# Performance work log

Measured on AMD Instinct MI355X. Metric: run time of the kernel, lower is better.

## Reference

```python
import jax, jax.numpy as jnp
import numpy as np

HEADS = 4
CH = 64  # hidden_channels (per-head out channels)
N_INT = 50000
N_LANE = 400000
E_PO = 400000
E_ADJ = 200000


def setup_inputs() -> dict:
    key = jax.random.key(0)
    ks = iter(jax.random.split(key, 32))
    rn = lambda shape, s=0.1: jax.random.normal(next(ks), shape, dtype=jnp.float32) * s
    inp = {
        'x_int': rn((N_INT, 16), 1.0),
        'x_lane': rn((N_LANE, 12), 1.0),
        'h0': jnp.zeros((N_INT, CH), jnp.float32),
        'enc_int_W': rn((16, CH)), 'enc_int_b': jnp.zeros((CH,), jnp.float32),
        'enc_lane_W': rn((12, CH)), 'enc_lane_b': jnp.zeros((CH,), jnp.float32),
        'Wsrc_po': rn((CH, HEADS * CH)), 'Wdst_po': rn((CH, HEADS * CH)),
        'att_src_po': rn((HEADS, CH)), 'att_dst_po': rn((HEADS, CH)),
        'bias_po': jnp.zeros((HEADS * CH,), jnp.float32),
        'Wsrc_adj': rn((CH, HEADS * CH)), 'Wdst_adj': rn((CH, HEADS * CH)),
        'att_src_adj': rn((HEADS, CH)), 'att_dst_adj': rn((HEADS, CH)),
        'bias_adj': jnp.zeros((HEADS * CH,), jnp.float32),
        'gru_W_ih': rn((3 * CH, HEADS * CH)), 'gru_W_hh': rn((3 * CH, CH)),
        'gru_b_ih': jnp.zeros((3 * CH,), jnp.float32), 'gru_b_hh': jnp.zeros((3 * CH,), jnp.float32),
        'W_pi': rn((CH, 8)), 'b_pi': jnp.zeros((8,), jnp.float32),
        'W_v': rn((CH, 1)), 'b_v': jnp.zeros((1,), jnp.float32),
        'src_po': jax.random.randint(next(ks), (E_PO,), 0, N_LANE),
        'dst_po': jax.random.randint(next(ks), (E_PO,), 0, N_INT),
        'src_adj': jax.random.randint(next(ks), (E_ADJ,), 0, N_INT),
        'dst_adj': jax.random.randint(next(ks), (E_ADJ,), 0, N_INT),
    }
    return inp


def gat_conv(x_src, x_dst, src, dst, Wsrc, Wdst, a_src, a_dst, bias, n_dst):
    # PyG GATConv (bipartite, concat=True, no self loops), negative_slope=0.2
    hs = (x_src @ Wsrc).reshape(-1, HEADS, CH)  # [Ns,H,C]
    hd = (x_dst @ Wdst).reshape(-1, HEADS, CH)  # [Nd,H,C]
    a_s = jnp.einsum('nhc,hc->nh', hs, a_src)   # [Ns,H]
    a_d = jnp.einsum('nhc,hc->nh', hd, a_dst)   # [Nd,H]
    alpha = jax.nn.leaky_relu(a_s[src] + a_d[dst], 0.2)        # [E,H]
    amax = jax.ops.segment_max(alpha, dst, num_segments=n_dst)  # [Nd,H]
    ex = jnp.exp(alpha - amax[dst])
    den = jax.ops.segment_sum(ex, dst, num_segments=n_dst)
    w = ex / den[dst]                                           # [E,H] softmax per dst
    msg = hs[src] * w[:, :, None]                               # [E,H,C]
    out = jax.ops.segment_sum(msg, dst, num_segments=n_dst)     # [Nd,H,C]
    return out.reshape(n_dst, HEADS * CH) + bias


def gru_cell(x, h, W_ih, W_hh, b_ih, b_hh):
    gi = x @ W_ih.T + b_ih
    gh = h @ W_hh.T + b_hh
    i_r, i_z, i_n = jnp.split(gi, 3, axis=1)
    h_r, h_z, h_n = jnp.split(gh, 3, axis=1)
    r = jax.nn.sigmoid(i_r + h_r)
    z = jax.nn.sigmoid(i_z + h_z)
    n = jnp.tanh(i_n + r * h_n)
    return (1.0 - z) * n + z * h


def reference(x_int, x_lane, h0, enc_int_W, enc_int_b, enc_lane_W, enc_lane_b,
              Wsrc_po, Wdst_po, att_src_po, att_dst_po, bias_po,
              Wsrc_adj, Wdst_adj, att_src_adj, att_dst_adj, bias_adj,
              gru_W_ih, gru_W_hh, gru_b_ih, gru_b_hh,
              W_pi, b_pi, W_v, b_v,
              src_po, dst_po, src_adj, dst_adj):
    # per-type encoders + ReLU
    e_int = jax.nn.relu(x_int @ enc_int_W + enc_int_b)    # [N_int,CH]
    e_lane = jax.nn.relu(x_lane @ enc_lane_W + enc_lane_b)  # [N_lane,CH]
    # HeteroConv aggr='sum' over relations targeting 'intersection'
    o_po = gat_conv(e_lane, e_int, src_po, dst_po, Wsrc_po, Wdst_po,
                    att_src_po, att_dst_po, bias_po, N_INT)
    o_adj = gat_conv(e_int, e_int, src_adj, dst_adj, Wsrc_adj, Wdst_adj,
                     att_src_adj, att_dst_adj, bias_adj, N_INT)
    inter = jax.nn.relu(o_po + o_adj)  # dropout = identity (deterministic eval)
    h_new = gru_cell(inter, h0, gru_W_ih, gru_W_hh, gru_b_ih, gru_b_hh)
    logits = h_new @ W_pi + b_pi
    value = h_new @ W_v + b_v
    return logits, value, h_new
```

## Files before the change

kernel.cpp:

```cpp
#include <hip/hip_runtime.h>

#define NI 50000
#define NL 400000
#define EPO 400000
#define EADJ 200000

#define K1_ITER 4
#define K2_ITER 4
#define K1_ROWS (32*K1_ITER)
#define K2_ROWS (32*K2_ITER)
#define NLB ((NL + K1_ROWS - 1)/K1_ROWS)
#define NIB ((NI + K2_ROWS - 1)/K2_ROWS)

typedef unsigned int u32;
typedef unsigned short u16;
typedef short bf16x8 __attribute__((ext_vector_type(8)));
typedef float f32x4 __attribute__((ext_vector_type(4)));

__device__ __forceinline__ float bf2f(u16 h){ return __uint_as_float(((u32)h)<<16); }
__device__ __forceinline__ u16 f2bf(float f){
  u32 u = __float_as_uint(f);
  u += 0x7FFFu + ((u>>16)&1u);
  return (u16)(u>>16);
}
__device__ __forceinline__ u32 pack2(float a, float b){
  return (u32)f2bf(a) | ((u32)f2bf(b)<<16);
}

__device__ __forceinline__ float b2_val(
    const float* __restrict__ W_ih, const float* __restrict__ W_hh, int m, int k)
{
  if(k < 256){ return (m<192) ? W_ih[m*256+k] : 0.f; }
  int kk = k-256;
  if(m<128) return W_hh[m*64+kk];
  if(m>=192) return W_hh[(m-64)*64+kk];
  return 0.f;
}

__global__ __launch_bounds__(256) void k0_prep(
    const float* __restrict__ Wsrc_po, const float* __restrict__ att_src_po,
    const float* __restrict__ Wdst_po, const float* __restrict__ att_dst_po,
    const float* __restrict__ Wsrc_adj, const float* __restrict__ att_src_adj,
    const float* __restrict__ Wdst_adj, const float* __restrict__ att_dst_adj,
    const float* __restrict__ W_ih, const float* __restrict__ W_hh,
    const float* __restrict__ bias_po, const float* __restrict__ bias_adj,
    const float* __restrict__ b_ih, const float* __restrict__ b_hh,
    float* __restrict__ v4, u16* __restrict__ WheadT, u16* __restrict__ B2F,
    float* __restrict__ bias_comb, float* __restrict__ bias2,
    int* __restrict__ cnt)
{
  const int T0 = 1024, T1 = 4*64*128, T2 = 10*16*64*8;
  const int TC = 2*NI;
  int total = T0 + T1 + T2 + 256 + 256 + TC;
  for(int t = blockIdx.x*256 + threadIdx.x; t < total; t += gridDim.x*256){
    if(t < T0){
      int which = t>>8, hc = t&255, h = hc>>6, c = hc&63;
      const float *W, *att;
      if(which==0){ W=Wsrc_po;  att=att_src_po; }
      else if(which==1){ W=Wdst_po;  att=att_dst_po; }
      else if(which==2){ W=Wsrc_adj; att=att_src_adj; }
      else { W=Wdst_adj; att=att_dst_adj; }
      float s=0.f;
      for(int j=0;j<64;j++) s += W[c*256 + h*64 + j]*att[h*64+j];
      v4[which*256 + hc] = s;
    } else if(t < T0 + T1){
      int i = t - T0; int h = i>>13, rem = i&8191, m = rem>>7, k = rem&127;
      float val = (k<64) ? Wsrc_po[k*256 + h*64 + m]
                         : Wsrc_adj[(k-64)*256 + h*64 + m];
      WheadT[i] = f2bf(val);
    } else if(t < T0 + T1 + T2){
      int i = t - (T0+T1);
      int j = i&7;
      int u4 = i>>3;
      int kstep = u4>>10, rem = u4&1023, tile = rem>>6, lane = rem&63;
      int col = tile*16 + (lane&15);
      int k = kstep*32 + (lane>>4)*8 + j;
      B2F[i] = f2bf(b2_val(W_ih, W_hh, col, k));
    } else if(t < T0 + T1 + T2 + 256){
      int m = t - (T0+T1+T2);
      bias_comb[m] = bias_po[m] + bias_adj[m];
    } else if(t < T0 + T1 + T2 + 512){
      int m = t - (T0+T1+T2+256);
      float v;
      if(m<128) v = b_ih[m] + b_hh[m];
      else if(m<192) v = b_ih[m];
      else v = b_hh[m-64];
      bias2[m] = v;
    } else {
      cnt[t - (T0+T1+T2+512)] = 0;
    }
  }
}

__global__ __launch_bounds__(256) void k_enc(
    const float* __restrict__ x_lane, const float* __restrict__ Wl, const float* __restrict__ bl,
    const float* __restrict__ x_int,  const float* __restrict__ Wi, const float* __restrict__ bi,
    const float* __restrict__ v_sp, const float* __restrict__ v_dp,
    const float* __restrict__ v_sa, const float* __restrict__ v_da,
    u16* __restrict__ e_lane, float* __restrict__ a_s_po,
    u16* __restrict__ e_int, float* __restrict__ a_dp, float* __restrict__ a_sa,
    float* __restrict__ a_da)
{
  int t = threadIdx.x;
  int wv = t>>6, l = t&63;
  int g = l&7, m = l>>3;
  int blk = blockIdx.x;
  if(blk < NLB){
    float wreg[12][8], breg[8];
#pragma unroll
    for(int k=0;k<12;k++){
      float4 w0 = *(const float4*)(Wl + k*64 + g*8);
      float4 w1 = *(const float4*)(Wl + k*64 + g*8 + 4);
      wreg[k][0]=w0.x; wreg[k][1]=w0.y; wreg[k][2]=w0.z; wreg[k][3]=w0.w;
      wreg[k][4]=w1.x; wreg[k][5]=w1.y; wreg[k][6]=w1.z; wreg[k][7]=w1.w;
    }
    {
      float4 b0 = *(const float4*)(bl + g*8);
      float4 b1 = *(const float4*)(bl + g*8 + 4);
      breg[0]=b0.x; breg[1]=b0.y; breg[2]=b0.z; breg[3]=b0.w;
      breg[4]=b1.x; breg[5]=b1.y; breg[6]=b1.z; breg[7]=b1.w;
    }
    int rowbase = blk*K1_ROWS + wv*(8*K1_ITER) + m;
    int row = rowbase;
    float4 xa={0,0,0,0}, xb={0,0,0,0}, xc={0,0,0,0};
    if(row < NL){
      const float4* xp = (const float4*)(x_lane + (size_t)row*12);
      xa = xp[0]; xb = xp[1]; xc = xp[2];
    }
#pragma unroll
    for(int it=0; it<K1_ITER; it++){
      int nrow = row + 8;
      float4 na={0,0,0,0}, nb={0,0,0,0}, nc={0,0,0,0};
      if(it+1 < K1_ITER && nrow < NL){
        const float4* xp = (const float4*)(x_lane + (size_t)nrow*12);
        na = xp[0]; nb = xp[1]; nc = xp[2];
      }
      float xv[12];
      xv[0]=xa.x; xv[1]=xa.y; xv[2]=xa.z; xv[3]=xa.w;
      xv[4]=xb.x; xv[5]=xb.y; xv[6]=xb.z; xv[7]=xb.w;
      xv[8]=xc.x; xv[9]=xc.y; xv[10]=xc.z; xv[11]=xc.w;
      float acc[8];
#pragma unroll
      for(int j=0;j<8;j++) acc[j]=breg[j];
#pragma unroll
      for(int k=0;k<12;k++){
        float xk = xv[k];
#pragma unroll
        for(int j=0;j<8;j++) acc[j] += xk*wreg[k][j];
      }
      float e[8];
#pragma unroll
      for(int j=0;j<8;j++) e[j] = fmaxf(acc[j], 0.f);
      float as[4];
#pragma unroll
      for(int h=0;h<4;h++){
        float4 v0 = *(const float4*)(v_sp + h*64 + g*8);
        float4 v1 = *(const float4*)(v_sp + h*64 + g*8 + 4);
        as[h] = e[0]*v0.x + e[1]*v0.y + e[2]*v0.z + e[3]*v0.w
              + e[4]*v1.x + e[5]*v1.y + e[6]*v1.z + e[7]*v1.w;
      }
#pragma unroll
      for(int o=1;o<8;o<<=1){
#pragma unroll
        for(int h=0;h<4;h++) as[h] += __shfl_xor(as[h], o, 64);
      }
      if(row < NL){
        uint4 P;
        P.x = pack2(e[0],e[1]); P.y = pack2(e[2],e[3]);
        P.z = pack2(e[4],e[5]); P.w = pack2(e[6],e[7]);
        ((uint4*)e_lane)[(size_t)row*8 + g] = P;
        if(g==0){
          float4 A; A.x=as[0]; A.y=as[1]; A.z=as[2]; A.w=as[3];
          *(float4*)(a_s_po + (size_t)row*4) = A;
        }
      }
      xa=na; xb=nb; xc=nc;
      row = nrow;
    }
  } else {
    int b2 = blk - NLB;
    float breg[8];
    {
      float4 b0 = *(const float4*)(bi + g*8);
      float4 b1 = *(const float4*)(bi + g*8 + 4);
      breg[0]=b0.x; breg[1]=b0.y; breg[2]=b0.z; breg[3]=b0.w;
      breg[4]=b1.x; breg[5]=b1.y; breg[6]=b1.z; breg[7]=b1.w;
    }
    int rowbase = b2*K2_ROWS + wv*(8*K2_ITER) + m;
#pragma unroll
    for(int it=0; it<K2_ITER; it++){
      int row = rowbase + it*8;
      float xv[16];
      if(row < NI){
        const float4* xp = (const float4*)(x_int + (size_t)row*16);
#pragma unroll
        for(int q=0;q<4;q++){
          float4 xq = xp[q];
          xv[q*4]=xq.x; xv[q*4+1]=xq.y; xv[q*4+2]=xq.z; xv[q*4+3]=xq.w;
        }
      } else {
#pragma unroll
        for(int k=0;k<16;k++) xv[k]=0.f;
      }
      float acc[8];
#pragma unroll
      for(int j=0;j<8;j++) acc[j]=breg[j];
#pragma unroll
      for(int k=0;k<16;k++){
        float4 w0 = *(const float4*)(Wi + k*64 + g*8);
        float4 w1 = *(const float4*)(Wi + k*64 + g*8 + 4);
        float xk = xv[k];
        acc[0] += xk*w0.x; acc[1] += xk*w0.y; acc[2] += xk*w0.z; acc[3] += xk*w0.w;
        acc[4] += xk*w1.x; acc[5] += xk*w1.y; acc[6] += xk*w1.z; acc[7] += xk*w1.w;
      }
      float e[8];
#pragma unroll
      for(int j=0;j<8;j++) e[j] = fmaxf(acc[j], 0.f);
      float ad[4], sa[4], da[4];
#pragma unroll
      for(int h=0;h<4;h++){
        float4 v0, v1;
        v0 = *(const float4*)(v_dp + h*64 + g*8); v1 = *(const float4*)(v_dp + h*64 + g*8 + 4);
        ad[h] = e[0]*v0.x + e[1]*v0.y + e[2]*v0.z + e[3]*v0.w
              + e[4]*v1.x + e[5]*v1.y + e[6]*v1.z + e[7]*v1.w;
        v0 = *(const float4*)(v_sa + h*64 + g*8); v1 = *(const float4*)(v_sa + h*64 + g*8 + 4);
        sa[h] = e[0]*v0.x + e[1]*v0.y + e[2]*v0.z + e[3]*v0.w
              + e[4]*v1.x + e[5]*v1.y + e[6]*v1.z + e[7]*v1.w;
        v0 = *(const float4*)(v_da + h*64 + g*8); v1 = *(const float4*)(v_da + h*64 + g*8 + 4);
        da[h] = e[0]*v0.x + e[1]*v0.y + e[2]*v0.z + e[3]*v0.w
              + e[4]*v1.x + e[5]*v1.y + e[6]*v1.z + e[7]*v1.w;
      }
#pragma unroll
      for(int o=1;o<8;o<<=1){
#pragma unroll
        for(int h=0;h<4;h++){
          ad[h] += __shfl_xor(ad[h], o, 64);
          sa[h] += __shfl_xor(sa[h], o, 64);
          da[h] += __shfl_xor(da[h], o, 64);
        }
      }
      if(row < NI){
        uint4 P;
        P.x = pack2(e[0],e[1]); P.y = pack2(e[2],e[3]);
        P.z = pack2(e[4],e[5]); P.w = pack2(e[6],e[7]);
        ((uint4*)e_int)[(size_t)row*8 + g] = P;
        if(g==0){
          float4 A;
          A.x=ad[0]; A.y=ad[1]; A.z=ad[2]; A.w=ad[3]; *(float4*)(a_dp + (size_t)row*4) = A;
          A.x=sa[0]; A.y=sa[1]; A.z=sa[2]; A.w=sa[3]; *(float4*)(a_sa + (size_t)row*4) = A;
          A.x=da[0]; A.y=da[1]; A.z=da[2]; A.w=da[3]; *(float4*)(a_da + (size_t)row*4) = A;
        }
      }
    }
  }
}

__global__ __launch_bounds__(256) void k3_hist(
    const int* __restrict__ dst_po, const int* __restrict__ dst_adj, int* __restrict__ cnt)
{
  int i = blockIdx.x*256 + threadIdx.x;
  if(i < EPO) atomicAdd(&cnt[dst_po[i]], 1);
  else if(i < EPO+EADJ) atomicAdd(&cnt[NI + dst_adj[i-EPO]], 1);
}

__global__ __launch_bounds__(1024) void k4a_scan(
    const int* __restrict__ cnt, int* __restrict__ offA, int* __restrict__ bsum)
{
  __shared__ int s[1024];
  int y = blockIdx.y;
  int i = blockIdx.x*1024 + threadIdx.x;
  int v = (i<NI) ? cnt[y*NI+i] : 0;
  s[threadIdx.x]=v;
  __syncthreads();
  for(int o=1;o<1024;o<<=1){
    int t = (threadIdx.x>=o) ? s[threadIdx.x-o] : 0;
    __syncthreads();
    s[threadIdx.x] += t;
    __syncthreads();
  }
  if(i<NI) offA[y*NI+i] = s[threadIdx.x]-v;
  if(threadIdx.x==1023) bsum[y*64+blockIdx.x] = s[1023];
}

__global__ __launch_bounds__(128) void k4b_scanb(int* __restrict__ bsum)
{
  int y = threadIdx.x>>6, lane = threadIdx.x&63;
  int v = (lane<49) ? bsum[y*64+lane] : 0;
  int orig = v;
#pragma unroll
  for(int o=1;o<64;o<<=1){
    int t = __shfl_up(v,o,64);
    if(lane>=o) v += t;
  }
  if(lane<49) bsum[y*64+lane] = v-orig;
}

__global__ __launch_bounds__(1024) void k4c_add(
    int* __restrict__ offA, int* __restrict__ cur, const int* __restrict__ bsum)
{
  int y = blockIdx.y;
  int i = blockIdx.x*1024 + threadIdx.x;
  if(i<NI){
    int o = offA[y*NI+i] + bsum[y*64+blockIdx.x];
    offA[y*NI+i]=o;
    cur[y*NI+i]=o;
  }
}

__global__ __launch_bounds__(256) void k5_scatter(
    const int* __restrict__ src_po, const int* __restrict__ dst_po,
    const int* __restrict__ src_adj, const int* __restrict__ dst_adj,
    const float* __restrict__ a_s_po, const float* __restrict__ a_d_po,
    const float* __restrict__ a_s_adj, const float* __restrict__ a_d_adj,
    int* __restrict__ cur, int* __restrict__ csr_po, int* __restrict__ csr_adj,
    float* __restrict__ pw_po, float* __restrict__ pw_adj)
{
  int i = blockIdx.x*256 + threadIdx.x;
  if(i < EPO){
    int s = src_po[i];
    int d = dst_po[i];
    int p = atomicAdd(&cur[d],1);
    csr_po[p] = s;
    float4 as = *(const float4*)(a_s_po + (size_t)s*4);
    float4 ad = *(const float4*)(a_d_po + (size_t)d*4);
    float4 pv;
    float x;
    x = as.x+ad.x; pv.x = __expf(x>0.f?x:0.2f*x);
    x = as.y+ad.y; pv.y = __expf(x>0.f?x:0.2f*x);
    x = as.z+ad.z; pv.z = __expf(x>0.f?x:0.2f*x);
    x = as.w+ad.w; pv.w = __expf(x>0.f?x:0.2f*x);
    *(float4*)(pw_po + (size_t)p*4) = pv;
  } else if(i < EPO+EADJ){
    int e = i-EPO;
    int s = src_adj[e];
    int d = dst_adj[e];
    int p = atomicAdd(&cur[NI+d],1);
    csr_adj[p] = s;
    float4 as = *(const float4*)(a_s_adj + (size_t)s*4);
    float4 ad = *(const float4*)(a_d_adj + (size_t)d*4);
    float4 pv;
    float x;
    x = as.x+ad.x; pv.x = __expf(x>0.f?x:0.2f*x);
    x = as.y+ad.y; pv.y = __expf(x>0.f?x:0.2f*x);
    x = as.z+ad.z; pv.z = __expf(x>0.f?x:0.2f*x);
    x = as.w+ad.w; pv.w = __expf(x>0.f?x:0.2f*x);
    *(float4*)(pw_adj + (size_t)p*4) = pv;
  }
}

__device__ __forceinline__ void agg_rel(
    int beg, int n, int lane,
    const int* __restrict__ csr, const float* __restrict__ pw,
    const u16* __restrict__ emat, u16* __restrict__ aggrow)
{
  float l0=0,l1=0,l2=0,l3=0;
  float c0=0,c1=0,c2=0,c3=0;
  for(int base=0;base<n;base+=64){
    int m = n-base; if(m>64) m=64;
    int sv_ = (lane<m) ? csr[beg+base+lane] : 0;
    int t2=0;
    for(; t2+1<m; t2+=2){
      int s0 = __shfl(sv_, t2, 64);
      int s1 = __shfl(sv_, t2+1, 64);
      float4 p0 = *(const float4*)(pw + (size_t)(beg+base+t2)*4);
      float4 p1 = *(const float4*)(pw + (size_t)(beg+base+t2+1)*4);
      float e0 = bf2f(emat[(size_t)s0*64+lane]);
      float e1 = bf2f(emat[(size_t)s1*64+lane]);
      c0 += p0.x*e0; c1 += p0.y*e0; c2 += p0.z*e0; c3 += p0.w*e0;
      l0 += p0.x;    l1 += p0.y;    l2 += p0.z;    l3 += p0.w;
      c0 += p1.x*e1; c1 += p1.y*e1; c2 += p1.z*e1; c3 += p1.w*e1;
      l0 += p1.x;    l1 += p1.y;    l2 += p1.z;    l3 += p1.w;
    }
    if(t2<m){
      int s0 = __shfl(sv_, t2, 64);
      float4 p0 = *(const float4*)(pw + (size_t)(beg+base+t2)*4);
      float e0 = bf2f(emat[(size_t)s0*64+lane]);
      c0 += p0.x*e0; c1 += p0.y*e0; c2 += p0.z*e0; c3 += p0.w*e0;
      l0 += p0.x;    l1 += p0.y;    l2 += p0.z;    l3 += p0.w;
    }
  }
  aggrow[lane]       = f2bf(n>0 ? c0/l0 : 0.f);
  aggrow[64+lane]    = f2bf(n>0 ? c1/l1 : 0.f);
  aggrow[128+lane]   = f2bf(n>0 ? c2/l2 : 0.f);
  aggrow[192+lane]   = f2bf(n>0 ? c3/l3 : 0.f);
}

__global__ __launch_bounds__(256) void k6_agg(
    const int* __restrict__ off, const int* __restrict__ cnt,
    const int* __restrict__ csr_po, const int* __restrict__ csr_adj,
    const float* __restrict__ pw_po, const float* __restrict__ pw_adj,
    const u16* __restrict__ e_lane, const u16* __restrict__ e_int,
    u16* __restrict__ agg)
{
  int wave=threadIdx.x>>6, lane=threadIdx.x&63;
  int d = blockIdx.x*4 + wave;
  if(d>=NI) return;
  agg_rel(off[d],    cnt[d],    lane, csr_po,  pw_po,  e_lane, agg + (size_t)d*512);
  agg_rel(off[NI+d], cnt[NI+d], lane, csr_adj, pw_adj, e_int,  agg + (size_t)d*512 + 256);
}

__global__ __launch_bounds__(256) void gemm_head(
    const u16* __restrict__ agg, const u16* __restrict__ WheadT,
    const float* __restrict__ bias, u16* __restrict__ inter256)
{
  __shared__ u16 As[64][136];
  __shared__ u16 Bs[64][136];
  int t=threadIdx.x, wave=t>>6, lane=t&63;
  int h = blockIdx.y;
  int row0 = blockIdx.x*64;
  int r = lane&15, q = lane>>4;
  const uint4* Bsrc = (const uint4*)(WheadT + (size_t)h*8192);
#pragma unroll
  for(int it=0; it<4; it++){
    int idx = it*256 + t;
    int brow = idx>>4, u4 = idx&15;
    *(uint4*)&Bs[brow][u4*8] = Bsrc[idx];
    int grow = row0 + brow;
    uint4 v = {0,0,0,0};
    if(grow < NI){
      int co = (u4<8) ? (h*64 + u4*8) : (256 + h*64 + (u4-8)*8);
      v = *(const uint4*)(agg + (size_t)grow*512 + co);
    }
    *(uint4*)&As[brow][u4*8] = v;
  }
  __syncthreads();
  f32x4 acc0={0,0,0,0}, acc1={0,0,0,0}, acc2={0,0,0,0}, acc3={0,0,0,0};
#pragma unroll
  for(int ks=0; ks<4; ks++){
    bf16x8 af = *(const bf16x8*)&As[wave*16 + r][q*8 + ks*32];
    bf16x8 b0 = *(const bf16x8*)&Bs[ 0 + r][q*8 + ks*32];
    bf16x8 b1 = *(const bf16x8*)&Bs[16 + r][q*8 + ks*32];
    bf16x8 b2 = *(const bf16x8*)&Bs[32 + r][q*8 + ks*32];
    bf16x8 b3 = *(const bf16x8*)&Bs[48 + r][q*8 + ks*32];
    acc0 = __builtin_amdgcn_mfma_f32_16x16x32_bf16(af,b0,acc0,0,0,0);
    acc1 = __builtin_amdgcn_mfma_f32_16x16x32_bf16(af,b1,acc1,0,0,0);
    acc2 = __builtin_amdgcn_mfma_f32_16x16x32_bf16(af,b2,acc2,0,0,0);
    acc3 = __builtin_amdgcn_mfma_f32_16x16x32_bf16(af,b3,acc3,0,0,0);
  }
  int crow_base = row0 + wave*16 + q*4;
#pragma unroll
  for(int t2=0;t2<4;t2++){
    f32x4 a = (t2==0)?acc0 : (t2==1)?acc1 : (t2==2)?acc2 : acc3;
    int col = h*64 + t2*16 + r;
    float bcol = bias[col];
#pragma unroll
    for(int rr=0;rr<4;rr++){
      int row = crow_base + rr;
      if(row < NI)
        inter256[(size_t)row*256 + col] = f2bf(fmaxf(a[rr]+bcol, 0.f));
    }
  }
}

__global__ __launch_bounds__(256) void k9_gru(
    const u16* __restrict__ inter256, const uint4* __restrict__ B2F,
    const float* __restrict__ bias2, const float* __restrict__ h0,
    const float* __restrict__ Wpi, const float* __restrict__ bpi,
    const float* __restrict__ Wv, const float* __restrict__ bvp,
    float* __restrict__ out)
{
  int t=threadIdx.x, w=t>>6, lane=t&63;
  int r = lane&15, q = lane>>4;
  int row0 = blockIdx.x*64;
  int arow = row0 + w*16 + r;
  int arc = arow < NI ? arow : NI-1;
  const u16* Aptr = inter256 + (size_t)arc*256 + q*8;
  const float* h0r = h0 + (size_t)arc*64 + q*8;
  f32x4 acc[16];
#pragma unroll
  for(int i=0;i<16;i++) acc[i] = (f32x4){0,0,0,0};
#pragma unroll
  for(int ks=0; ks<10; ks++){
    bf16x8 af;
    if(ks < 8){
      af = *(const bf16x8*)(Aptr + ks*32);
    } else {
      const float* hp = h0r + (ks-8)*32;
      float4 f0 = *(const float4*)(hp);
      float4 f1 = *(const float4*)(hp+4);
      uint4 P;
      P.x = pack2(f0.x,f0.y); P.y = pack2(f0.z,f0.w);
      P.z = pack2(f1.x,f1.y); P.w = pack2(f1.z,f1.w);
      *(uint4*)&af = P;
    }
    const uint4* bp = B2F + ks*1024 + lane;
#pragma unroll
    for(int tt=0;tt<16;tt++){
      uint4 bu = bp[tt*64];
      bf16x8 bf; *(uint4*)&bf = bu;
      acc[tt] = __builtin_amdgcn_mfma_f32_16x16x32_bf16(af, bf, acc[tt], 0,0,0);
    }
  }
  float pk[4][8];
  float pv[4];
#pragma unroll
  for(int rr=0;rr<4;rr++){
    pv[rr]=0.f;
#pragma unroll
    for(int j=0;j<8;j++) pk[rr][j]=0.f;
  }
  int rbase = row0 + w*16 + q*4;
#pragma unroll
  for(int t2=0;t2<4;t2++){
    int c = t2*16 + r;
    float b0 = bias2[c], b1 = bias2[64+c], b2 = bias2[128+c], b3 = bias2[192+c];
    float wp[8];
#pragma unroll
    for(int j=0;j<8;j++) wp[j] = Wpi[c*8+j];
    float wv = Wv[c];
#pragma unroll
    for(int rr=0;rr<4;rr++){
      int row = rbase + rr;
      float g0 = acc[t2][rr]    + b0;
      float g1 = acc[t2+4][rr]  + b1;
      float g2 = acc[t2+8][rr]  + b2;
      float g3 = acc[t2+12][rr] + b3;
      float h0v = (row < NI) ? h0[(size_t)row*64 + c] : 0.f;
      float rg = 1.f/(1.f+__expf(-g0));
      float zg = 1.f/(1.f+__expf(-g1));
      float e2 = __expf(2.f*(g2 + rg*g3));
      float ng = 1.f - 2.f/(e2+1.f);
      float h = (1.f-zg)*ng + zg*h0v;
      if(row < NI) out[450000 + (size_t)row*64 + c] = h;
#pragma unroll
      for(int j=0;j<8;j++) pk[rr][j] += h*wp[j];
      pv[rr] += h*wv;
    }
  }
#pragma unroll
  for(int o=1;o<16;o<<=1){
#pragma unroll
    for(int rr=0;rr<4;rr++){
#pragma unroll
      for(int j=0;j<8;j++) pk[rr][j] += __shfl_xor(pk[rr][j], o, 64);
      pv[rr] += __shfl_xor(pv[rr], o, 64);
    }
  }
  if(r==0){
#pragma unroll
    for(int rr=0;rr<4;rr++){
      int row = rbase + rr;
      if(row < NI){
#pragma unroll
        for(int j=0;j<8;j++) out[(size_t)row*8 + j] = pk[rr][j] + bpi[j];
        out[400000 + row] = pv[rr] + bvp[0];
      }
    }
  }
}

extern "C" void kernel_launch(void* const* d_in, const int* in_sizes, int n_in,
                              void* d_out, int out_size, void* d_ws, size_t ws_size,
                              hipStream_t stream) {
  const float* x_int      = (const float*)d_in[0];
  const float* x_lane     = (const float*)d_in[1];
  const float* h0         = (const float*)d_in[2];
  const float* enc_int_W  = (const float*)d_in[3];
  const float* enc_int_b  = (const float*)d_in[4];
  const float* enc_lane_W = (const float*)d_in[5];
  const float* enc_lane_b = (const float*)d_in[6];
  const float* Wsrc_po    = (const float*)d_in[7];
  const float* Wdst_po    = (const float*)d_in[8];
  const float* att_src_po = (const float*)d_in[9];
  const float* att_dst_po = (const float*)d_in[10];
  const float* bias_po    = (const float*)d_in[11];
  const float* Wsrc_adj   = (const float*)d_in[12];
  const float* Wdst_adj   = (const float*)d_in[13];
  const float* att_src_adj= (const float*)d_in[14];
  const float* att_dst_adj= (const float*)d_in[15];
  const float* bias_adj   = (const float*)d_in[16];
  const float* gru_W_ih   = (const float*)d_in[17];
  const float* gru_W_hh   = (const float*)d_in[18];
  const float* gru_b_ih   = (const float*)d_in[19];
  const float* gru_b_hh   = (const float*)d_in[20];
  const float* W_pi       = (const float*)d_in[21];
  const float* b_pi       = (const float*)d_in[22];
  const float* W_v        = (const float*)d_in[23];
  const float* b_v        = (const float*)d_in[24];
  const int* src_po  = (const int*)d_in[25];
  const int* dst_po  = (const int*)d_in[26];
  const int* src_adj = (const int*)d_in[27];
  const int* dst_adj = (const int*)d_in[28];
  float* out = (float*)d_out;

  char* w = (char*)d_ws;
  size_t ofs = 0;
  auto alloc = [&](size_t bytes)->char*{
    char* p = w + ofs;
    ofs = (ofs + bytes + 255) & ~(size_t)255;
    return p;
  };
  u16*  e_lane   = (u16*)alloc((size_t)NL*64*2);
  u16*  e_int    = (u16*)alloc((size_t)NI*64*2);
  float* a_s_po  = (float*)alloc((size_t)NL*4*4);
  float* a_d_po  = (float*)alloc((size_t)NI*4*4);
  float* a_s_adj = (float*)alloc((size_t)NI*4*4);
  float* a_d_adj = (float*)alloc((size_t)NI*4*4);
  int*  cnt      = (int*)alloc((size_t)2*NI*4);
  int*  offA     = (int*)alloc((size_t)2*NI*4);
  int*  cur      = (int*)alloc((size_t)2*NI*4);
  int*  csr_po   = (int*)alloc((size_t)EPO*4);
  int*  csr_adj  = (int*)alloc((size_t)EADJ*4);
  float* pw_po   = (float*)alloc((size_t)EPO*4*4);
  float* pw_adj  = (float*)alloc((size_t)EADJ*4*4);
  int*  bsum     = (int*)alloc(2*64*4);
  u16*  agg      = (u16*)alloc((size_t)NI*512*2);
  u16*  inter256 = (u16*)alloc((size_t)NI*256*2);
  u16*  WheadT   = (u16*)alloc(4*64*128*2);
  u16*  B2F      = (u16*)alloc(10*16*64*8*2);
  float* v4      = (float*)alloc(4*256*4);
  float* bias_comb = (float*)alloc(256*4);
  float* bias2   = (float*)alloc(256*4);
  (void)ws_size; (void)n_in; (void)in_sizes; (void)out_size;

  k0_prep<<<256, 256, 0, stream>>>(
      Wsrc_po, att_src_po, Wdst_po, att_dst_po,
      Wsrc_adj, att_src_adj, Wdst_adj, att_dst_adj,
      gru_W_ih, gru_W_hh, bias_po, bias_adj, gru_b_ih, gru_b_hh,
      v4, WheadT, B2F, bias_comb, bias2, cnt);
  k_enc<<<NLB+NIB, 256, 0, stream>>>(
      x_lane, enc_lane_W, enc_lane_b,
      x_int, enc_int_W, enc_int_b,
      v4 + 0, v4 + 256, v4 + 512, v4 + 768,
      e_lane, a_s_po, e_int, a_d_po, a_s_adj, a_d_adj);
  k3_hist<<<(EPO+EADJ+255)/256, 256, 0, stream>>>(dst_po, dst_adj, cnt);
  k4a_scan<<<dim3(49,2), 1024, 0, stream>>>(cnt, offA, bsum);
  k4b_scanb<<<1, 128, 0, stream>>>(bsum);
  k4c_add<<<dim3(49,2), 1024, 0, stream>>>(offA, cur, bsum);
  k5_scatter<<<(EPO+EADJ+255)/256, 256, 0, stream>>>(src_po, dst_po, src_adj, dst_adj,
      a_s_po, a_d_po, a_s_adj, a_d_adj,
      cur, csr_po, csr_adj, pw_po, pw_adj);
  k6_agg<<<(NI+3)/4, 256, 0, stream>>>(offA, cnt, csr_po, csr_adj,
      pw_po, pw_adj, e_lane, e_int, agg);
  gemm_head<<<dim3((NI+63)/64, 4), 256, 0, stream>>>(agg, WheadT, bias_comb, inter256);
  k9_gru<<<(NI+63)/64, 256, 0, stream>>>(inter256, (const uint4*)B2F, bias2, h0,
      W_pi, b_pi, W_v, b_v, out);
}
```

Measured before the change: 376.7 us.

## Fold histogram into encoder kernel, split aggregation relations across waves, deepen prefetch

The edge-count histogram is merged into the encoder launch as extra blocks, which removes one kernel launch and lets the atomic traffic overlap with the encoder work. The aggregation kernel now uses 512 threads, so the two relations for each destination node run on separate waves instead of one after the other in a single wave. The lane encoder handles twice as many rows per block and prefetches inputs two iterations ahead. In exchange, register pressure in the encoder rises, and the separate waves no longer share work.

Result: no change. 371.8 us (-1.3%).

```diff
diff --git a/kernel.cpp b/kernel.cpp
--- a/kernel.cpp
+++ b/kernel.cpp
@@ -5,12 +5,13 @@
 #define EPO 400000
 #define EADJ 200000
 
-#define K1_ITER 4
+#define K1_ITER 8
 #define K2_ITER 4
 #define K1_ROWS (32*K1_ITER)
 #define K2_ROWS (32*K2_ITER)
 #define NLB ((NL + K1_ROWS - 1)/K1_ROWS)
 #define NIB ((NI + K2_ROWS - 1)/K2_ROWS)
+#define NHB ((EPO + EADJ + 255)/256)
 
 typedef unsigned int u32;
 typedef unsigned short u16;
@@ -99,7 +100,9 @@
     const float* __restrict__ v_sa, const float* __restrict__ v_da,
     u16* __restrict__ e_lane, float* __restrict__ a_s_po,
     u16* __restrict__ e_int, float* __restrict__ a_dp, float* __restrict__ a_sa,
-    float* __restrict__ a_da)
+    float* __restrict__ a_da,
+    const int* __restrict__ dst_po, const int* __restrict__ dst_adj,
+    int* __restrict__ cnt)
 {
   int t = threadIdx.x;
   int wv = t>>6, l = t&63;
@@ -121,24 +124,28 @@
       breg[4]=b1.x; breg[5]=b1.y; breg[6]=b1.z; breg[7]=b1.w;
     }
     int rowbase = blk*K1_ROWS + wv*(8*K1_ITER) + m;
-    int row = rowbase;
-    float4 xa={0,0,0,0}, xb={0,0,0,0}, xc={0,0,0,0};
-    if(row < NL){
-      const float4* xp = (const float4*)(x_lane + (size_t)row*12);
-      xa = xp[0]; xb = xp[1]; xc = xp[2];
+    float4 Aa={0,0,0,0}, Ab={0,0,0,0}, Ac={0,0,0,0};
+    float4 Ba={0,0,0,0}, Bb={0,0,0,0}, Bc={0,0,0,0};
+    if(rowbase < NL){
+      const float4* xp = (const float4*)(x_lane + (size_t)rowbase*12);
+      Aa = xp[0]; Ab = xp[1]; Ac = xp[2];
+    }
+    if(rowbase+8 < NL){
+      const float4* xp = (const float4*)(x_lane + (size_t)(rowbase+8)*12);
+      Ba = xp[0]; Bb = xp[1]; Bc = xp[2];
     }
 #pragma unroll
     for(int it=0; it<K1_ITER; it++){
-      int nrow = row + 8;
-      float4 na={0,0,0,0}, nb={0,0,0,0}, nc={0,0,0,0};
-      if(it+1 < K1_ITER && nrow < NL){
-        const float4* xp = (const float4*)(x_lane + (size_t)nrow*12);
-        na = xp[0]; nb = xp[1]; nc = xp[2];
+      int row = rowbase + it*8;
+      float4 Ca={0,0,0,0}, Cb={0,0,0,0}, Cc={0,0,0,0};
+      if(it+2 < K1_ITER && row+16 < NL){
+        const float4* xp = (const float4*)(x_lane + (size_t)(row+16)*12);
+        Ca = xp[0]; Cb = xp[1]; Cc = xp[2];
       }
       float xv[12];
-      xv[0]=xa.x; xv[1]=xa.y; xv[2]=xa.z; xv[3]=xa.w;
-      xv[4]=xb.x; xv[5]=xb.y; xv[6]=xb.z; xv[7]=xb.w;
-      xv[8]=xc.x; xv[9]=xc.y; xv[10]=xc.z; xv[11]=xc.w;
+      xv[0]=Aa.x; xv[1]=Aa.y; xv[2]=Aa.z; xv[3]=Aa.w;
+      xv[4]=Ab.x; xv[5]=Ab.y; xv[6]=Ab.z; xv[7]=Ab.w;
+      xv[8]=Ac.x; xv[9]=Ac.y; xv[10]=Ac.z; xv[11]=Ac.w;
       float acc[8];
 #pragma unroll
       for(int j=0;j<8;j++) acc[j]=breg[j];
@@ -174,10 +181,10 @@
           *(float4*)(a_s_po + (size_t)row*4) = A;
         }
       }
-      xa=na; xb=nb; xc=nc;
-      row = nrow;
-    }
-  } else {
+      Aa=Ba; Ab=Bb; Ac=Bc;
+      Ba=Ca; Bb=Cb; Bc=Cc;
+    }
+  } else if(blk < NLB + NIB){
     int b2 = blk - NLB;
     float breg[8];
     {
@@ -252,15 +259,11 @@
         }
       }
     }
-  }
-}
-
-__global__ __launch_bounds__(256) void k3_hist(
-    const int* __restrict__ dst_po, const int* __restrict__ dst_adj, int* __restrict__ cnt)
-{
-  int i = blockIdx.x*256 + threadIdx.x;
-  if(i < EPO) atomicAdd(&cnt[dst_po[i]], 1);
-  else if(i < EPO+EADJ) atomicAdd(&cnt[NI + dst_adj[i-EPO]], 1);
+  } else {
+    int i = (blk - NLB - NIB)*256 + t;
+    if(i < EPO) atomicAdd(&cnt[dst_po[i]], 1);
+    else if(i < EPO+EADJ) atomicAdd(&cnt[NI + dst_adj[i-EPO]], 1);
+  }
 }
 
 __global__ __launch_bounds__(1024) void k4a_scan(
@@ -385,7 +388,7 @@
   aggrow[192+lane]   = f2bf(n>0 ? c3/l3 : 0.f);
 }
 
-__global__ __launch_bounds__(256) void k6_agg(
+__global__ __launch_bounds__(512) void k6_agg(
     const int* __restrict__ off, const int* __restrict__ cnt,
     const int* __restrict__ csr_po, const int* __restrict__ csr_adj,
     const float* __restrict__ pw_po, const float* __restrict__ pw_adj,
@@ -393,10 +396,12 @@
     u16* __restrict__ agg)
 {
   int wave=threadIdx.x>>6, lane=threadIdx.x&63;
-  int d = blockIdx.x*4 + wave;
+  int d = blockIdx.x*4 + (wave&3);
   if(d>=NI) return;
-  agg_rel(off[d],    cnt[d],    lane, csr_po,  pw_po,  e_lane, agg + (size_t)d*512);
-  agg_rel(off[NI+d], cnt[NI+d], lane, csr_adj, pw_adj, e_int,  agg + (size_t)d*512 + 256);
+  if(wave < 4)
+    agg_rel(off[d],    cnt[d],    lane, csr_po,  pw_po,  e_lane, agg + (size_t)d*512);
+  else
+    agg_rel(off[NI+d], cnt[NI+d], lane, csr_adj, pw_adj, e_int,  agg + (size_t)d*512 + 256);
 }
 
 __global__ __launch_bounds__(256) void gemm_head(
@@ -618,19 +623,19 @@
       Wsrc_adj, att_src_adj, Wdst_adj, att_dst_adj,
       gru_W_ih, gru_W_hh, bias_po, bias_adj, gru_b_ih, gru_b_hh,
       v4, WheadT, B2F, bias_comb, bias2, cnt);
-  k_enc<<<NLB+NIB, 256, 0, stream>>>(
+  k_enc<<<NLB+NIB+NHB, 256, 0, stream>>>(
       x_lane, enc_lane_W, enc_lane_b,
       x_int, enc_int_W, enc_int_b,
       v4 + 0, v4 + 256, v4 + 512, v4 + 768,
-      e_lane, a_s_po, e_int, a_d_po, a_s_adj, a_d_adj);
-  k3_hist<<<(EPO+EADJ+255)/256, 256, 0, stream>>>(dst_po, dst_adj, cnt);
+      e_lane, a_s_po, e_int, a_d_po, a_s_adj, a_d_adj,
+      dst_po, dst_adj, cnt);
   k4a_scan<<<dim3(49,2), 1024, 0, stream>>>(cnt, offA, bsum);
   k4b_scanb<<<1, 128, 0, stream>>>(bsum);
   k4c_add<<<dim3(49,2), 1024, 0, stream>>>(offA, cur, bsum);
   k5_scatter<<<(EPO+EADJ+255)/256, 256, 0, stream>>>(src_po, dst_po, src_adj, dst_adj,
       a_s_po, a_d_po, a_s_adj, a_d_adj,
       cur, csr_po, csr_adj, pw_po, pw_adj);
-  k6_agg<<<(NI+3)/4, 256, 0, stream>>>(offA, cnt, csr_po, csr_adj,
+  k6_agg<<<(NI+3)/4, 512, 0, stream>>>(offA, cnt, csr_po, csr_adj,
       pw_po, pw_adj, e_lane, e_int, agg);
   gemm_head<<<dim3((NI+63)/64, 4), 256, 0, stream>>>(agg, WheadT, bias_comb, inter256);
   k9_gru<<<(NI+63)/64, 256, 0, stream>>>(inter256, (const uint4*)B2F, bias2, h0,
```
